# Kernel tuning notes

Hardware: AMD Instinct MI355X
Metric: run time of the kernel (lower is better)

Reference implementation:

```python
import jax, jax.numpy as jnp
import numpy as np

EPS = 1e-6  # torch.nn.PairwiseDistance default eps, added to the difference before norm
B, D, H, W = 2048, 1024, 128, 128


def setup_inputs() -> dict:
    key = jax.random.key(0)
    k1, k2 = jax.random.split(key)
    x = jax.random.normal(k1, (B, D), dtype=jnp.float32)
    # SOM codebook: [input_size, H*W], matches torch.randn(input_size, out_size[0]*out_size[1])
    weight = jax.random.normal(k2, (D, H * W), dtype=jnp.float32)
    # grid locations, row-major (x, y) as produced by get_map_index()
    gx, gy = jnp.meshgrid(jnp.arange(H), jnp.arange(W), indexing='ij')
    locations = jnp.stack([gx.ravel(), gy.ravel()], axis=1).astype(jnp.float32)  # [H*W, 2]
    return {"x": x, "weight": weight, "locations": locations}


def reference(x, weight, locations):
    # dists[b, m] = || x[b] - weight[:, m] + EPS ||_2  (PairwiseDistance p=2 semantics)
    d = x.shape[1]
    sq = (jnp.sum(x * x, axis=1, keepdims=True)          # [B, 1]
          + jnp.sum(weight * weight, axis=0)[None, :]    # [1, M]
          - 2.0 * (x @ weight)                            # [B, M] GEMM
          + 2.0 * EPS * (jnp.sum(x, axis=1, keepdims=True) - jnp.sum(weight, axis=0)[None, :])
          + d * EPS * EPS)
    dists = jnp.sqrt(jnp.maximum(sq, 0.0))                # [B, M]
    losses = jnp.min(dists, axis=1, keepdims=True)        # [B, 1]
    bmu_indexes = jnp.argmin(dists, axis=1, keepdims=True)  # [B, 1] int
    bmu_locations = locations[bmu_indexes]                 # [B, 1, 2]
    loss = jnp.sum(losses) / x.shape[0]                    # scalar mean min-distance
    return bmu_indexes, bmu_locations, loss
```

## Files before the change

### kernel.cpp

```cpp
#include <hip/hip_runtime.h>
#include <cstdint>
#include <cstddef>


#define B_  2048
#define D_  1024
#define M_  16384
#define EPS_ 1e-6f

typedef _Float16 v8h __attribute__((ext_vector_type(8)));
typedef _Float16 v4h __attribute__((ext_vector_type(4)));
typedef float    v4f __attribute__((ext_vector_type(4)));

static __device__ __forceinline__ unsigned long long umin64(unsigned long long a,
                                                            unsigned long long b) {
    return a < b ? a : b;
}

__global__ void xconv(const float* __restrict__ x,
                      _Float16* __restrict__ xh, _Float16* __restrict__ xl,
                      float* __restrict__ rowTerm) {
    int b = blockIdx.x;
    int t = threadIdx.x;
    const float4 v = *(const float4*)(x + (size_t)b * D_ + t * 4);
    v4h h, l;
    float acc = 0.f;
    float vv[4] = {v.x, v.y, v.z, v.w};
    #pragma unroll
    for (int e = 0; e < 4; ++e) {
        _Float16 hi = (_Float16)vv[e];
        float lo = vv[e] - (float)hi;
        h[e] = hi; l[e] = (_Float16)lo;
        acc += vv[e] * vv[e] + 2.0f * EPS_ * vv[e];
    }
    *(v4h*)(xh + (size_t)b * D_ + t * 4) = h;
    *(v4h*)(xl + (size_t)b * D_ + t * 4) = l;
    for (int off = 32; off; off >>= 1) acc += __shfl_down(acc, off, 64);
    __shared__ float s[4];
    if ((t & 63) == 0) s[t >> 6] = acc;
    __syncthreads();
    if (t == 0) rowTerm[b] = s[0] + s[1] + s[2] + s[3];
}

__global__ void wconv(const float* __restrict__ W,
                      _Float16* __restrict__ wth, _Float16* __restrict__ wtl,
                      float* __restrict__ colTerm) {
    __shared__ float tile[64][65];
    const int t = threadIdx.x;
    const int m0 = blockIdx.x * 64;
    const int d0 = blockIdx.y * 64;
    const int dloc = t >> 4, mq = (t & 15) * 4;
    #pragma unroll
    for (int s = 0; s < 4; ++s) {
        float4 v = *(const float4*)(W + (size_t)(d0 + dloc + 16 * s) * M_ + m0 + mq);
        tile[dloc + 16 * s][mq + 0] = v.x;
        tile[dloc + 16 * s][mq + 1] = v.y;
        tile[dloc + 16 * s][mq + 2] = v.z;
        tile[dloc + 16 * s][mq + 3] = v.w;
    }
    __syncthreads();
    const int mloc = t >> 2;
    const int dc = (t & 3) * 16;
    v8h h0, l0, h1, l1;
    float acc = 0.f;
    #pragma unroll
    for (int e = 0; e < 8; ++e) {
        float v = tile[dc + e][mloc];
        _Float16 hi = (_Float16)v;
        h0[e] = hi; l0[e] = (_Float16)(v - (float)hi);
        acc += v * v - 2.0f * EPS_ * v;
    }
    #pragma unroll
    for (int e = 0; e < 8; ++e) {
        float v = tile[dc + 8 + e][mloc];
        _Float16 hi = (_Float16)v;
        h1[e] = hi; l1[e] = (_Float16)(v - (float)hi);
        acc += v * v - 2.0f * EPS_ * v;
    }
    _Float16* oh = wth + (size_t)(m0 + mloc) * D_ + d0 + dc;
    _Float16* ol = wtl + (size_t)(m0 + mloc) * D_ + d0 + dc;
    *(v8h*)oh = h0; *(v8h*)(oh + 8) = h1;
    *(v8h*)ol = l0; *(v8h*)(ol + 8) = l1;
    acc += __shfl_xor(acc, 1, 64);
    acc += __shfl_xor(acc, 2, 64);
    if ((t & 3) == 0) atomicAdd(&colTerm[m0 + mloc], acc);
}

__global__ __launch_bounds__(256, 2) void som_mfma(
    const _Float16* __restrict__ xh, const _Float16* __restrict__ xl,
    const _Float16* __restrict__ wth, const _Float16* __restrict__ wtl,
    const float* __restrict__ rowTerm, const float* __restrict__ colTerm,
    unsigned long long* __restrict__ keys)
{
    __shared__ __align__(16) _Float16 smem[16384];
    _Float16* Ah = smem;
    _Float16* Al = smem + 4096;
    _Float16* Bh = smem + 8192;
    _Float16* Bl = smem + 12288;

    const int t  = threadIdx.x;
    const int rb = blockIdx.y * 128;
    const int cb = blockIdx.x * 128;
    const int L  = t & 63, w = t >> 6;
    const int wro = (w >> 1) * 64, wco = (w & 1) * 64;
    const int c16 = L & 15, kq = L >> 4;

    const size_t ga0 = (size_t)(rb + (t >> 2)) * 2048 + (t & 3) * 16;
    const size_t ga1 = ga0 + 64ull * 2048;
    const size_t gb0 = (size_t)(cb + (t >> 2)) * 2048 + (t & 3) * 16;
    const size_t gb1 = gb0 + 64ull * 2048;

    int fm = ((t >> 6) << 6) + ((t & 3) << 4) + ((t >> 2) & 15);
    const int ws0 = (fm ^ ((fm >> 3) & 7)) * 16;
    const int ws1 = ws0 + 4096;

    const char* pxh = (const char*)xh;
    const char* pxl = (const char*)xl;
    const char* pwh = (const char*)wth;
    const char* pwl = (const char*)wtl;

    v4f acc[4][4];
    #pragma unroll
    for (int i = 0; i < 4; ++i)
        #pragma unroll
        for (int j = 0; j < 4; ++j) acc[i][j] = (v4f){0.f, 0.f, 0.f, 0.f};

    const int Lswz = (L & 56) + ((L & 7) ^ ((L >> 3) & 7));
    int ia[4], ib[4];
    #pragma unroll
    for (int i = 0; i < 4; ++i) {
        ia[i] = (((wro >> 4) + i) * 64 + Lswz) * 8;
        ib[i] = (((wco >> 4) + i) * 64 + Lswz) * 8;
    }

    float4 rA0h = *(const float4*)(pxh + ga0);
    float4 rA1h = *(const float4*)(pxh + ga1);
    float4 rA0l = *(const float4*)(pxl + ga0);
    float4 rA1l = *(const float4*)(pxl + ga1);
    float4 rB0h = *(const float4*)(pwh + gb0);
    float4 rB1h = *(const float4*)(pwh + gb1);
    float4 rB0l = *(const float4*)(pwl + gb0);
    float4 rB1l = *(const float4*)(pwl + gb1);
    *(float4*)((char*)Ah + ws0) = rA0h;  *(float4*)((char*)Ah + ws1) = rA1h;
    *(float4*)((char*)Al + ws0) = rA0l;  *(float4*)((char*)Al + ws1) = rA1l;
    *(float4*)((char*)Bh + ws0) = rB0h;  *(float4*)((char*)Bh + ws1) = rB1h;
    *(float4*)((char*)Bl + ws0) = rB0l;  *(float4*)((char*)Bl + ws1) = rB1l;
    __syncthreads();

    for (int kb = 64; kb <= 2048; kb += 64) {
        const bool more = (kb < 2048);
        if (more) {
            rA0h = *(const float4*)(pxh + ga0 + kb);
            rA1h = *(const float4*)(pxh + ga1 + kb);
            rA0l = *(const float4*)(pxl + ga0 + kb);
            rA1l = *(const float4*)(pxl + ga1 + kb);
            rB0h = *(const float4*)(pwh + gb0 + kb);
            rB1h = *(const float4*)(pwh + gb1 + kb);
            rB0l = *(const float4*)(pwl + gb0 + kb);
            rB1l = *(const float4*)(pwl + gb1 + kb);
        }

        v8h ah[4], al4[4], bh4[4], bl4[4];
        #pragma unroll
        for (int i = 0; i < 4; ++i) {
            ah[i]  = *(const v8h*)(Ah + ia[i]);
            al4[i] = *(const v8h*)(Al + ia[i]);
            bh4[i] = *(const v8h*)(Bh + ib[i]);
            bl4[i] = *(const v8h*)(Bl + ib[i]);
        }
        #pragma unroll
        for (int i = 0; i < 4; ++i)
            #pragma unroll
            for (int j = 0; j < 4; ++j) {
                acc[i][j] = __builtin_amdgcn_mfma_f32_16x16x32_f16(ah[i],  bh4[j], acc[i][j], 0, 0, 0);
                acc[i][j] = __builtin_amdgcn_mfma_f32_16x16x32_f16(ah[i],  bl4[j], acc[i][j], 0, 0, 0);
                acc[i][j] = __builtin_amdgcn_mfma_f32_16x16x32_f16(al4[i], bh4[j], acc[i][j], 0, 0, 0);
            }

        __syncthreads();
        if (more) {
            *(float4*)((char*)Ah + ws0) = rA0h;  *(float4*)((char*)Ah + ws1) = rA1h;
            *(float4*)((char*)Al + ws0) = rA0l;  *(float4*)((char*)Al + ws1) = rA1l;
            *(float4*)((char*)Bh + ws0) = rB0h;  *(float4*)((char*)Bh + ws1) = rB1h;
            *(float4*)((char*)Bl + ws0) = rB0l;  *(float4*)((char*)Bl + ws1) = rB1l;
        }
        __syncthreads();
    }

    float cT[4];
    #pragma unroll
    for (int j = 0; j < 4; ++j) cT[j] = colTerm[cb + wco + j * 16 + c16];
    const float de2 = (float)D_ * EPS_ * EPS_;
    #pragma unroll
    for (int i = 0; i < 4; ++i) {
        #pragma unroll
        for (int r = 0; r < 4; ++r) {
            int row_g = rb + wro + i * 16 + kq * 4 + r;
            float rt = rowTerm[row_g];
            unsigned long long best = ~0ull;
            #pragma unroll
            for (int j = 0; j < 4; ++j) {
                float sq = rt + cT[j] - 2.0f * acc[i][j][r] + de2;
                sq = fmaxf(sq, 0.0f);
                float dist = sqrtf(sq);
                unsigned long long key =
                    ((unsigned long long)__float_as_uint(dist) << 32) |
                    (unsigned int)(cb + wco + j * 16 + c16);
                best = umin64(best, key);
            }
            #pragma unroll
            for (int m = 1; m <= 8; m <<= 1) {
                unsigned long long o =
                    (unsigned long long)__shfl_xor((long long)best, m, 64);
                best = umin64(best, o);
            }
            if (c16 == 0) atomicMin(&keys[row_g], best);
        }
    }
}

__global__ void row_stats(const float* __restrict__ x, float* __restrict__ rowTerm) {
    int b = blockIdx.x;
    const float* xr = x + (size_t)b * D_;
    int t = threadIdx.x;
    float acc = 0.f;
    for (int i = t; i < D_; i += 256) {
        float v = xr[i];
        acc += v * v + 2.0f * EPS_ * v;
    }
    for (int off = 32; off; off >>= 1) acc += __shfl_down(acc, off, 64);
    __shared__ float s[4];
    if ((t & 63) == 0) s[t >> 6] = acc;
    __syncthreads();
    if (t == 0) rowTerm[b] = s[0] + s[1] + s[2] + s[3];
}

__global__ void col_stats(const float* __restrict__ w, float* __restrict__ colTerm) {
    int m = blockIdx.x * 256 + threadIdx.x;
    int d0 = blockIdx.y * 64;
    const float* p = w + (size_t)d0 * M_ + m;
    float acc = 0.f;
    #pragma unroll 8
    for (int d = 0; d < 64; ++d) {
        float v = p[(size_t)d * M_];
        acc += v * v - 2.0f * EPS_ * v;
    }
    atomicAdd(&colTerm[m], acc);
}

__global__ __launch_bounds__(256, 2) void som_gemm(
    const float* __restrict__ A, const float* __restrict__ Wt,
    const float* __restrict__ rowTerm, const float* __restrict__ colTerm,
    unsigned long long* __restrict__ keys)
{
    __shared__ float As[8][128];
    __shared__ float Bs[8][128];
    const int t  = threadIdx.x;
    const int rb = blockIdx.y * 128;
    const int cb = blockIdx.x * 128;
    const int tx = t & 15;
    const int ty = t >> 4;
    float acc[8][8];
    #pragma unroll
    for (int i = 0; i < 8; ++i)
        #pragma unroll
        for (int j = 0; j < 8; ++j) acc[i][j] = 0.f;
    const int la_row = t >> 1, la_k = (t & 1) * 4;
    const int lb_k = t >> 5, lb_n = (t & 31) * 4;
    const float* Aptr = A + (size_t)(rb + la_row) * D_ + la_k;
    const float* Bptr = Wt + (size_t)lb_k * M_ + cb + lb_n;
    for (int k0 = 0; k0 < D_; k0 += 8) {
        float4 av = *(const float4*)(Aptr + k0);
        float4 bv = *(const float4*)(Bptr + (size_t)k0 * M_);
        __syncthreads();
        As[la_k + 0][la_row] = av.x;
        As[la_k + 1][la_row] = av.y;
        As[la_k + 2][la_row] = av.z;
        As[la_k + 3][la_row] = av.w;
        *(float4*)&Bs[lb_k][lb_n] = bv;
        __syncthreads();
        #pragma unroll
        for (int k = 0; k < 8; ++k) {
            float a[8], b[8];
            #pragma unroll
            for (int i = 0; i < 8; ++i) a[i] = As[k][ty * 8 + i];
            #pragma unroll
            for (int j = 0; j < 8; ++j) b[j] = Bs[k][tx * 8 + j];
            #pragma unroll
            for (int i = 0; i < 8; ++i)
                #pragma unroll
                for (int j = 0; j < 8; ++j) acc[i][j] += a[i] * b[j];
        }
    }
    float rT[8], cT[8];
    #pragma unroll
    for (int i = 0; i < 8; ++i) rT[i] = rowTerm[rb + ty * 8 + i];
    #pragma unroll
    for (int j = 0; j < 8; ++j) cT[j] = colTerm[cb + tx * 8 + j];
    const float de2 = (float)D_ * EPS_ * EPS_;
    #pragma unroll
    for (int i = 0; i < 8; ++i) {
        unsigned long long best = ~0ull;
        #pragma unroll
        for (int j = 0; j < 8; ++j) {
            float sq = rT[i] + cT[j] - 2.0f * acc[i][j] + de2;
            sq = fmaxf(sq, 0.0f);
            float dist = sqrtf(sq);
            unsigned long long key =
                ((unsigned long long)__float_as_uint(dist) << 32) |
                (unsigned int)(cb + tx * 8 + j);
            best = umin64(best, key);
        }
        #pragma unroll
        for (int msk = 1; msk <= 8; msk <<= 1) {
            unsigned long long o = __shfl_xor((long long)best, msk, 64);
            best = umin64(best, (unsigned long long)o);
        }
        if (tx == 0) atomicMin(&keys[rb + ty * 8 + i], best);
    }
}

__global__ void finalize(const unsigned long long* __restrict__ keys,
                         const float* __restrict__ loc,
                         float* __restrict__ out)
{
    int t = threadIdx.x;
    int r = blockIdx.x * 256 + t;
    unsigned long long k = keys[r];
    unsigned int idx = (unsigned int)(k & 0xFFFFFFFFu);
    float dist = __uint_as_float((unsigned int)(k >> 32));
    out[r] = (float)idx;
    out[B_ + 2 * r]     = loc[2 * idx];
    out[B_ + 2 * r + 1] = loc[2 * idx + 1];
    float sum = dist;
    for (int off = 32; off; off >>= 1) sum += __shfl_down(sum, off, 64);
    __shared__ float s[4];
    if ((t & 63) == 0) s[t >> 6] = sum;
    __syncthreads();
    if (t == 0) atomicAdd(&out[3 * B_], (s[0] + s[1] + s[2] + s[3]) / (float)B_);
}

extern "C" void kernel_launch(void* const* d_in, const int* in_sizes, int n_in,
                              void* d_out, int out_size, void* d_ws, size_t ws_size,
                              hipStream_t stream)
{
    const float* x   = (const float*)d_in[0];
    const float* w   = (const float*)d_in[1];
    const float* loc = (const float*)d_in[2];
    float* out = (float*)d_out;

    char* ws = (char*)d_ws;
    unsigned long long* keys = (unsigned long long*)ws;
    float* rowTerm = (float*)(ws + (16 << 10));
    float* colTerm = (float*)(ws + (24 << 10));
    _Float16* xh  = (_Float16*)(ws + (1ull << 20));
    _Float16* xl  = (_Float16*)(ws + (5ull << 20));
    _Float16* wth = (_Float16*)(ws + (9ull << 20));
    _Float16* wtl = (_Float16*)(ws + (41ull << 20));
    const size_t NEED = 73ull << 20;

    hipMemsetAsync(keys, 0xFF, B_ * sizeof(unsigned long long), stream);
    hipMemsetAsync(colTerm, 0, M_ * sizeof(float), stream);
    hipMemsetAsync(out + 3 * B_, 0, sizeof(float), stream);

    if (ws_size >= NEED) {
        xconv<<<B_, 256, 0, stream>>>(x, xh, xl, rowTerm);
        wconv<<<dim3(M_ / 64, D_ / 64), 256, 0, stream>>>(w, wth, wtl, colTerm);
        som_mfma<<<dim3(M_ / 128, B_ / 128), 256, 0, stream>>>(
            xh, xl, wth, wtl, rowTerm, colTerm, keys);
    } else {
        row_stats<<<B_, 256, 0, stream>>>(x, rowTerm);
        col_stats<<<dim3(M_ / 256, D_ / 64), 256, 0, stream>>>(w, colTerm);
        som_gemm<<<dim3(M_ / 128, B_ / 128), 256, 0, stream>>>(
            x, w, rowTerm, colTerm, keys);
    }
    finalize<<<8, 256, 0, stream>>>(keys, loc, out);
}
```

Measured before the change: 354.8 us.

## Double-buffer LDS tiles in MFMA GEMM and group blocks for L2 reuse

Splits shared memory into two buffers. The next k-chunk is written to the idle buffer while the current one is consumed by the MFMAs, which drops one barrier per 64-wide k step. It also flattens the grid and remaps block ids so groups of 16 column tiles sweep all row tiles together, aiming to improve L2 reuse of the codebook. LDS use per block doubles to 64KB. The prefetch reads one chunk past the end of each row, and the workspace requirement is enlarged to cover the final overrun.

```diff
diff --git a/kernel.cpp b/kernel.cpp
--- a/kernel.cpp
+++ b/kernel.cpp
@@ -92,15 +92,14 @@
     const float* __restrict__ rowTerm, const float* __restrict__ colTerm,
     unsigned long long* __restrict__ keys)
 {
-    __shared__ __align__(16) _Float16 smem[16384];
-    _Float16* Ah = smem;
-    _Float16* Al = smem + 4096;
-    _Float16* Bh = smem + 8192;
-    _Float16* Bl = smem + 12288;
+    __shared__ __align__(16) _Float16 smem[32768];
 
     const int t  = threadIdx.x;
-    const int rb = blockIdx.y * 128;
-    const int cb = blockIdx.x * 128;
+    const int g   = blockIdx.x;
+    const int grp = g >> 8, loc = g & 255;
+    const int cb  = ((grp << 4) + (loc & 15)) * 128;
+    const int rb  = (loc >> 4) * 128;
+
     const int L  = t & 63, w = t >> 6;
     const int wro = (w >> 1) * 64, wco = (w & 1) * 64;
     const int c16 = L & 15, kq = L >> 4;
@@ -133,57 +132,77 @@
         ib[i] = (((wco >> 4) + i) * 64 + Lswz) * 8;
     }
 
-    float4 rA0h = *(const float4*)(pxh + ga0);
-    float4 rA1h = *(const float4*)(pxh + ga1);
-    float4 rA0l = *(const float4*)(pxl + ga0);
-    float4 rA1l = *(const float4*)(pxl + ga1);
-    float4 rB0h = *(const float4*)(pwh + gb0);
-    float4 rB1h = *(const float4*)(pwh + gb1);
-    float4 rB0l = *(const float4*)(pwl + gb0);
-    float4 rB1l = *(const float4*)(pwl + gb1);
-    *(float4*)((char*)Ah + ws0) = rA0h;  *(float4*)((char*)Ah + ws1) = rA1h;
-    *(float4*)((char*)Al + ws0) = rA0l;  *(float4*)((char*)Al + ws1) = rA1l;
-    *(float4*)((char*)Bh + ws0) = rB0h;  *(float4*)((char*)Bh + ws1) = rB1h;
-    *(float4*)((char*)Bl + ws0) = rB0l;  *(float4*)((char*)Bl + ws1) = rB1l;
+    float4 rA0h, rA1h, rA0l, rA1l, rB0h, rB1h, rB0l, rB1l;
+
+    #define LOAD_REGS(kb)                                                       \
+        do {                                                                    \
+            rA0h = *(const float4*)(pxh + ga0 + (kb));                          \
+            rA1h = *(const float4*)(pxh + ga1 + (kb));                          \
+            rA0l = *(const float4*)(pxl + ga0 + (kb));                          \
+            rA1l = *(const float4*)(pxl + ga1 + (kb));                          \
+            rB0h = *(const float4*)(pwh + gb0 + (kb));                          \
+            rB1h = *(const float4*)(pwh + gb1 + (kb));                          \
+            rB0l = *(const float4*)(pwl + gb0 + (kb));                          \
+            rB1l = *(const float4*)(pwl + gb1 + (kb));                          \
+        } while (0)
+
+    #define WRITE_LDS(base)                                                     \
+        do {                                                                    \
+            char* Ahb = (char*)(base);                                          \
+            *(float4*)(Ahb + ws0)          = rA0h;                              \
+            *(float4*)(Ahb + ws1)          = rA1h;                              \
+            *(float4*)(Ahb + 8192 + ws0)   = rA0l;                              \
+            *(float4*)(Ahb + 8192 + ws1)   = rA1l;                              \
+            *(float4*)(Ahb + 16384 + ws0)  = rB0h;                              \
+            *(float4*)(Ahb + 16384 + ws1)  = rB1h;                              \
+            *(float4*)(Ahb + 24576 + ws0)  = rB0l;                              \
+            *(float4*)(Ahb + 24576 + ws1)  = rB1l;                              \
+        } while (0)
+
+    #define COMPUTE(base)                                                       \
+        do {                                                                    \
+            const _Float16* Ahp = (base);                                       \
+            const _Float16* Alp = (base) + 4096;                                \
+            const _Float16* Bhp = (base) + 8192;                                \
+            const _Float16* Blp = (base) + 12288;                               \
+            v8h ah[4], al4[4], bh4[4], bl4[4];                                  \
+            _Pragma("unroll")                                                   \
+            for (int i = 0; i < 4; ++i) {                                       \
+                ah[i]  = *(const v8h*)(Ahp + ia[i]);                            \
+                al4[i] = *(const v8h*)(Alp + ia[i]);                            \
+                bh4[i] = *(const v8h*)(Bhp + ib[i]);                            \
+                bl4[i] = *(const v8h*)(Blp + ib[i]);                            \
+            }                                                                   \
+            _Pragma("unroll")                                                   \
+            for (int i = 0; i < 4; ++i)                                         \
+                _Pragma("unroll")                                               \
+                for (int j = 0; j < 4; ++j) {                                   \
+                    acc[i][j] = __builtin_amdgcn_mfma_f32_16x16x32_f16(         \
+                        ah[i],  bh4[j], acc[i][j], 0, 0, 0);                    \
+                    acc[i][j] = __builtin_amdgcn_mfma_f32_16x16x32_f16(         \
+                        ah[i],  bl4[j], acc[i][j], 0, 0, 0);                    \
+                    acc[i][j] = __builtin_amdgcn_mfma_f32_16x16x32_f16(         \
+                        al4[i], bh4[j], acc[i][j], 0, 0, 0);                    \
+                }                                                               \
+        } while (0)
+
+    _Float16* buf0 = smem;
+    _Float16* buf1 = smem + 16384;
+
+    LOAD_REGS(0);
+    WRITE_LDS(buf0);
+    LOAD_REGS(64);
     __syncthreads();
 
-    for (int kb = 64; kb <= 2048; kb += 64) {
-        const bool more = (kb < 2048);
-        if (more) {
-            rA0h = *(const float4*)(pxh + ga0 + kb);
-            rA1h = *(const float4*)(pxh + ga1 + kb);
-            rA0l = *(const float4*)(pxl + ga0 + kb);
-            rA1l = *(const float4*)(pxl + ga1 + kb);
-            rB0h = *(const float4*)(pwh + gb0 + kb);
-            rB1h = *(const float4*)(pwh + gb1 + kb);
-            rB0l = *(const float4*)(pwl + gb0 + kb);
-            rB1l = *(const float4*)(pwl + gb1 + kb);
-        }
-
-        v8h ah[4], al4[4], bh4[4], bl4[4];
-        #pragma unroll
-        for (int i = 0; i < 4; ++i) {
-            ah[i]  = *(const v8h*)(Ah + ia[i]);
-            al4[i] = *(const v8h*)(Al + ia[i]);
-            bh4[i] = *(const v8h*)(Bh + ib[i]);
-            bl4[i] = *(const v8h*)(Bl + ib[i]);
-        }
-        #pragma unroll
-        for (int i = 0; i < 4; ++i)
-            #pragma unroll
-            for (int j = 0; j < 4; ++j) {
-                acc[i][j] = __builtin_amdgcn_mfma_f32_16x16x32_f16(ah[i],  bh4[j], acc[i][j], 0, 0, 0);
-                acc[i][j] = __builtin_amdgcn_mfma_f32_16x16x32_f16(ah[i],  bl4[j], acc[i][j], 0, 0, 0);
-                acc[i][j] = __builtin_amdgcn_mfma_f32_16x16x32_f16(al4[i], bh4[j], acc[i][j], 0, 0, 0);
-            }
-
+    for (int kb = 0; kb < 2048; kb += 128) {
+        WRITE_LDS(buf1);
+        LOAD_REGS(kb + 128);
+        COMPUTE(buf0);
         __syncthreads();
-        if (more) {
-            *(float4*)((char*)Ah + ws0) = rA0h;  *(float4*)((char*)Ah + ws1) = rA1h;
-            *(float4*)((char*)Al + ws0) = rA0l;  *(float4*)((char*)Al + ws1) = rA1l;
-            *(float4*)((char*)Bh + ws0) = rB0h;  *(float4*)((char*)Bh + ws1) = rB1h;
-            *(float4*)((char*)Bl + ws0) = rB0l;  *(float4*)((char*)Bl + ws1) = rB1l;
-        }
+
+        WRITE_LDS(buf0);
+        LOAD_REGS(kb + 192);
+        COMPUTE(buf1);
         __syncthreads();
     }
 
@@ -217,6 +236,9 @@
             if (c16 == 0) atomicMin(&keys[row_g], best);
         }
     }
+    #undef LOAD_REGS
+    #undef WRITE_LDS
+    #undef COMPUTE
 }
 
 __global__ void row_stats(const float* __restrict__ x, float* __restrict__ rowTerm) {
@@ -357,7 +379,7 @@
     _Float16* xl  = (_Float16*)(ws + (5ull << 20));
     _Float16* wth = (_Float16*)(ws + (9ull << 20));
     _Float16* wtl = (_Float16*)(ws + (41ull << 20));
-    const size_t NEED = 73ull << 20;
+    const size_t NEED = 74ull << 20;
 
     hipMemsetAsync(keys, 0xFF, B_ * sizeof(unsigned long long), stream);
     hipMemsetAsync(colTerm, 0, M_ * sizeof(float), stream);
@@ -366,7 +388,7 @@
     if (ws_size >= NEED) {
         xconv<<<B_, 256, 0, stream>>>(x, xh, xl, rowTerm);
         wconv<<<dim3(M_ / 64, D_ / 64), 256, 0, stream>>>(w, wth, wtl, colTerm);
-        som_mfma<<<dim3(M_ / 128, B_ / 128), 256, 0, stream>>>(
+        som_mfma<<<2048, 256, 0, stream>>>(
             xh, xl, wth, wtl, rowTerm, colTerm, keys);
     } else {
         row_stats<<<B_, 256, 0, stream>>>(x, rowTerm);
```

Result: faster. 344.3 us (-2.9%).
